# Kernel optimization log

Hardware: AMD Instinct MI355X
Metric: run time of the kernel (lower is better)

## Reference

```python
import jax, jax.numpy as jnp
import numpy as np

SEQ, BATCH, IN_DIM, HID, LAYERS, OUT = 512, 64, 512, 1024, 4, 1


def setup_inputs() -> dict:
    key = jax.random.key(0)
    ks = jax.random.split(key, 8)
    s = 1.0 / np.sqrt(HID)  # PyTorch default init range
    u = lambda k, shape: jax.random.uniform(k, shape, jnp.float32, -s, s)
    return {
        "x": jax.random.normal(ks[0], (SEQ, BATCH, IN_DIM), jnp.float32),
        "w_ih0": u(ks[1], (4 * HID, IN_DIM)),
        "w_ih_rest": u(ks[2], (LAYERS - 1, 4 * HID, HID)),
        "w_hh": u(ks[3], (LAYERS, 4 * HID, HID)),
        "b_ih": u(ks[4], (LAYERS, 4 * HID)),
        "b_hh": u(ks[5], (LAYERS, 4 * HID)),
        "fc_w": u(ks[6], (OUT, HID)),
        "fc_b": u(ks[7], (OUT,)),
    }


def _lstm_layer(xs, w_ih, w_hh, b):
    # xs: [T, B, D]; PyTorch gate order: i, f, g, o
    T, B, _ = xs.shape
    H = w_hh.shape[1]
    gx = jnp.einsum("tbd,gd->tbg", xs, w_ih) + b  # precompute input GEMM [T,B,4H]

    def step(carry, g_t):
        h, c = carry
        g = g_t + h @ w_hh.T
        i, f, gg, o = jnp.split(g, 4, axis=-1)
        c = jax.nn.sigmoid(f) * c + jax.nn.sigmoid(i) * jnp.tanh(gg)
        h = jax.nn.sigmoid(o) * jnp.tanh(c)
        return (h, c), h

    init = (jnp.zeros((B, H), xs.dtype), jnp.zeros((B, H), xs.dtype))
    _, hs = jax.lax.scan(step, init, gx)
    return hs  # [T, B, H]


def reference(x, w_ih0, w_ih_rest, w_hh, b_ih, b_hh, fc_w, fc_b):
    h = _lstm_layer(x, w_ih0, w_hh[0], b_ih[0] + b_hh[0])
    for l in range(1, LAYERS):
        h = _lstm_layer(h, w_ih_rest[l - 1], w_hh[l], b_ih[l] + b_hh[l])
    # Faithful to original: output is seq-first [T,B,H], and x[:, -1, :]
    # selects the LAST BATCH element over all timesteps -> [T, H]
    last = jax.nn.sigmoid(h[:, -1, :])
    return last @ fc_w.T + fc_b  # [T, OUT]
```

## Files before the change

### kernel.cpp

```cpp
#include <hip/hip_runtime.h>


typedef unsigned short u16;
typedef short bf16x8 __attribute__((ext_vector_type(8)));
typedef float f32x4 __attribute__((ext_vector_type(4)));
typedef float f32x16 __attribute__((ext_vector_type(16)));

__device__ __forceinline__ u16 f2bf(float f) {
  unsigned u = __float_as_uint(f);
  return (u16)((u + 0x7FFFu + ((u >> 16) & 1u)) >> 16);
}
__device__ __forceinline__ float bf2f(u16 s) {
  return __uint_as_float(((unsigned)s) << 16);
}
__device__ __forceinline__ bf16x8 ld8(const u16* p) {
  uint4 v = *(const uint4*)p;
  return __builtin_bit_cast(bf16x8, v);
}
__device__ __forceinline__ float sigf(float x) {
  x = fminf(fmaxf(x, -30.f), 30.f);
  return 1.f / (1.f + __expf(-x));
}
__device__ __forceinline__ float tanhf_(float x) {
  x = fminf(fmaxf(x, -15.f), 15.f);
  float e = __expf(-2.f * x);
  return (1.f - e) / (1.f + e);
}

#define AT_LD(p) __hip_atomic_load((p), __ATOMIC_RELAXED, __HIP_MEMORY_SCOPE_AGENT)
#define AT_ST(p, v) __hip_atomic_store((p), (v), __ATOMIC_RELAXED, __HIP_MEMORY_SCOPE_AGENT)

__global__ void repack_w(const float* __restrict__ wih0, const float* __restrict__ wihr,
                         const float* __restrict__ whh, u16* __restrict__ WCAT) {
  size_t i = (size_t)blockIdx.x * 256 + threadIdx.x;
  int l = (int)(i >> 23);
  int r = (int)(i >> 11) & 4095;
  int c = (int)i & 2047;
  int Kx = l ? 1024 : 512;
  float v = 0.f;
  if (c < Kx) v = l ? wihr[((size_t)(l - 1) * 4096 + r) * 1024 + c]
                    : wih0[(size_t)r * 512 + c];
  else if (c < Kx + 1024) v = whh[((size_t)l * 4096 + r) * 1024 + (c - Kx)];
  WCAT[i] = f2bf(v);
}

__global__ void repack_x(const float* __restrict__ x, u16* __restrict__ XP) {
  int i = blockIdx.x * 256 + threadIdx.x;
  int t = i >> 12, r = i & 4095, kc = r >> 6, b = r & 63;
  const float* src = x + ((size_t)t * 64 + b) * 512 + kc * 8;
  float4 v0 = *(const float4*)src, v1 = *(const float4*)(src + 4);
  u16 o[8] = {f2bf(v0.x), f2bf(v0.y), f2bf(v0.z), f2bf(v0.w),
              f2bf(v1.x), f2bf(v1.y), f2bf(v1.z), f2bf(v1.w)};
  *(uint4*)(XP + ((size_t)(t * 64 + kc) * 64 + b) * 8) = *(uint4*)o;
}

__global__ void bias_add(const float* __restrict__ a, const float* __restrict__ b,
                         float* __restrict__ o) {
  int i = blockIdx.x * blockDim.x + threadIdx.x;
  o[i] = a[i] + b[i];
}

template <int NF, int FX>
__device__ __forceinline__ void run_pipe(
    int layer, int w64, const u16* __restrict__ WCAT, const u16* __restrict__ XP,
    u16* __restrict__ HR, u16* __restrict__ HOUT, const float* __restrict__ BIAS,
    int* __restrict__ FLAG, float* R) {
  const int tid = threadIdx.x;
  const int lane = tid & 63, wv = tid >> 6;
  const int ks = wv & 3, nh = wv >> 2;
  const int l31 = lane & 31, lhi = lane >> 5;
  const int W = layer * 64 + w64;

  bf16x8 wf[NF];
  {
    const int lr = nh * 32 + l31;
    const int grow = (lr >> 4) * 1024 + 16 * w64 + (lr & 15);
    const u16* wrow = WCAT + ((size_t)layer * 4096 + grow) * 2048;
#pragma unroll
    for (int kk = 0; kk < NF; ++kk) {
      int f = ks * NF + kk;
      wf[kk] = ld8(wrow + f * 16 + lhi * 8);
    }
  }

  const int u = tid & 15, bp = tid >> 4;
  const int col = 16 * w64 + u;
  float c0 = 0.f, c1 = 0.f;
  const float bi = BIAS[layer * 4096 + col];
  const float bf_ = BIAS[layer * 4096 + 1024 + col];
  const float bg = BIAS[layer * 4096 + 2048 + col];
  const float bo = BIAS[layer * 4096 + 3072 + col];

  const int lane_base = (lhi * 64 + l31) * 8;
  u16* HRL = HR + (size_t)layer * 2097152;
  const u16* M0B = (NF == 32) ? HR + (size_t)(layer - 1) * 2097152 : XP;
  const int lrD = nh * 32 + l31;

  const bool needA = (layer > 0) && (ks * NF < FX);
  const bool needB = (ks * NF + NF > FX);
  const bool needC = (layer < 3);
  const int lm1 = (layer > 0) ? layer - 1 : layer;
  const int lp1 = (layer < 3) ? layer + 1 : layer;
  int* fA = FLAG + (lm1 * 64 + lane) * 64;
  int* fB = FLAG + (layer * 64 + lane) * 64;
  int* fC = FLAG + (lp1 * 64 + lane) * 64;
  const int NEVER = -0x40000000;

  *(f32x4*)&R[tid * 8] = f32x4{0.f, 0.f, 0.f, 0.f};
  *(f32x4*)&R[tid * 8 + 4] = f32x4{0.f, 0.f, 0.f, 0.f};
  __syncthreads();

  for (int t = 0; t < 512; ++t) {
    if (needC && (t & 7) == 0) {
      const int thC = t - 24;
      for (;;) {
        bool ok = AT_LD(fC) >= thC;
        if (__ballot(ok) == ~0ull) break;
      }
    }
    {
      const int thA = needA ? t + 1 : NEVER;
      const int thB = needB ? t : NEVER;
      for (;;) {
        bool ok = (AT_LD(fA) >= thA) & (AT_LD(fB) >= thB);
        if (__ballot(ok) == ~0ull) break;
      }
    }

    float* Rb = R + (t & 1) * 4096;
    const u16* P0 = M0B + ((NF == 32) ? (size_t)(t & 31) * 65536
                                      : (size_t)t * 32768) + lane_base;
    const u16* P1 = HRL + (size_t)((t - 1) & 31) * 65536 + lane_base - (size_t)FX * 1024;

    f32x16 acc0 = {}, acc1 = {};
    uint4 a0[8], a1[8];
#pragma unroll
    for (int p = 0; p < 8; ++p) {
      int f = ks * NF + p;
      const u16* ap = (f < FX ? P0 : P1) + (size_t)f * 1024;
      a0[p] = *(const uint4*)ap;
      a1[p] = *(const uint4*)(ap + 256);
    }
#pragma unroll
    for (int kk = 0; kk < NF; ++kk) {
      uint4 ca = a0[kk & 7], cb = a1[kk & 7];
      if (kk + 8 < NF) {
        int f = ks * NF + kk + 8;
        const u16* ap = (f < FX ? P0 : P1) + (size_t)f * 1024;
        a0[kk & 7] = *(const uint4*)ap;
        a1[kk & 7] = *(const uint4*)(ap + 256);
      }
      acc0 = __builtin_amdgcn_mfma_f32_32x32x16_bf16(
          __builtin_bit_cast(bf16x8, ca), wf[kk], acc0, 0, 0, 0);
      acc1 = __builtin_amdgcn_mfma_f32_32x32x16_bf16(
          __builtin_bit_cast(bf16x8, cb), wf[kk], acc1, 0, 0, 0);
    }
#pragma unroll
    for (int r = 0; r < 16; ++r) {
      int m = (r & 3) + 8 * (r >> 2) + 4 * lhi;
      atomicAdd(&Rb[m * 64 + lrD], acc0[r]);
      atomicAdd(&Rb[(32 + m) * 64 + lrD], acc1[r]);
    }
    __syncthreads();
    {
      float p0i = Rb[bp * 64 + u] + bi, p0f = Rb[bp * 64 + 16 + u] + bf_;
      float p0g = Rb[bp * 64 + 32 + u] + bg, p0o = Rb[bp * 64 + 48 + u] + bo;
      float p1i = Rb[(bp + 32) * 64 + u] + bi, p1f = Rb[(bp + 32) * 64 + 16 + u] + bf_;
      float p1g = Rb[(bp + 32) * 64 + 32 + u] + bg, p1o = Rb[(bp + 32) * 64 + 48 + u] + bo;
      c0 = sigf(p0f) * c0 + sigf(p0i) * tanhf_(p0g);
      float h0 = sigf(p0o) * tanhf_(c0);
      c1 = sigf(p1f) * c1 + sigf(p1i) * tanhf_(p1g);
      float h1 = sigf(p1o) * tanhf_(c1);
      u16 hb0 = f2bf(h0), hb1 = f2bf(h1);
      unsigned n0 = (unsigned)(u16)__shfl_down((int)(unsigned)hb0, 1, 64);
      unsigned n1 = (unsigned)(u16)__shfl_down((int)(unsigned)hb1, 1, 64);
      if ((u & 1) == 0) {
        unsigned pk0 = (unsigned)hb0 | (n0 << 16);
        unsigned pk1 = (unsigned)hb1 | (n1 << 16);
        u16* slot = HRL + (size_t)(t & 31) * 65536;
        size_t e0 = ((size_t)(col >> 3) * 64 + bp) * 8 + (col & 7);
        AT_ST((unsigned*)(slot + e0), pk0);
        AT_ST((unsigned*)(slot + e0 + 256), pk1);
        if (layer == 3 && bp == 31)
          *(unsigned*)(HOUT + (size_t)t * 1024 + col) = pk1;
      }
      float* Rn = R + ((t + 1) & 1) * 4096;
      *(f32x4*)&Rn[tid * 8] = f32x4{0.f, 0.f, 0.f, 0.f};
      *(f32x4*)&Rn[tid * 8 + 4] = f32x4{0.f, 0.f, 0.f, 0.f};
    }
    __syncthreads();
    if (tid == 0) AT_ST(&FLAG[W * 64], t + 1);
  }
}

__global__ __launch_bounds__(512, 2) void lstm_pipe(
    const u16* __restrict__ WCAT, const u16* __restrict__ XP,
    u16* __restrict__ HR, u16* __restrict__ HOUT,
    const float* __restrict__ BIAS, int* __restrict__ FLAG) {
  __shared__ float R[2 * 4096];
  const int w = blockIdx.x;
  const int layer = w >> 6, w64 = w & 63;
  if (layer == 0) run_pipe<24, 32>(0, w64, WCAT, XP, HR, HOUT, BIAS, FLAG, R);
  else            run_pipe<32, 64>(layer, w64, WCAT, XP, HR, HOUT, BIAS, FLAG, R);
}

__global__ void lstm_head(const u16* __restrict__ Hl, const float* __restrict__ fcw,
                          const float* __restrict__ fcb, float* __restrict__ out) {
  int t = blockIdx.x, tid = threadIdx.x;
  const u16* hrow = Hl + (size_t)t * 1024;
  float s = 0.f;
  for (int j = tid; j < 1024; j += 256)
    s += sigf(bf2f(hrow[j])) * fcw[j];
  for (int o = 32; o; o >>= 1) s += __shfl_down(s, o, 64);
  __shared__ float red[4];
  if ((tid & 63) == 0) red[tid >> 6] = s;
  __syncthreads();
  if (tid == 0) out[t] = red[0] + red[1] + red[2] + red[3] + fcb[0];
}

extern "C" void kernel_launch(void* const* d_in, const int* in_sizes, int n_in,
                              void* d_out, int out_size, void* d_ws, size_t ws_size,
                              hipStream_t stream) {
  const float* x    = (const float*)d_in[0];
  const float* wih0 = (const float*)d_in[1];
  const float* wihr = (const float*)d_in[2];
  const float* whh  = (const float*)d_in[3];
  const float* bih  = (const float*)d_in[4];
  const float* bhh  = (const float*)d_in[5];
  const float* fcw  = (const float*)d_in[6];
  const float* fcb  = (const float*)d_in[7];
  float* out = (float*)d_out;

  char* ws = (char*)d_ws;
  size_t off = 0;
  auto alc = [&](size_t b) { void* p = ws + off; off = (off + b + 255) & ~(size_t)255; return p; };
  u16* WCAT  = (u16*)alc(33554432ull * 2);
  u16* XP    = (u16*)alc(16777216ull * 2);
  u16* HR    = (u16*)alc(8388608ull * 2);
  u16* HOUT  = (u16*)alc(524288ull * 2);
  float* BIAS = (float*)alc(16384 * 4);
  int* FLAG  = (int*)alc(256 * 64 * 4);
  (void)ws_size; (void)in_sizes; (void)n_in; (void)out_size;

  hipMemsetAsync(HR, 0, 8388608ull * 2, stream);
  hipMemsetAsync(FLAG, 0, 256 * 64 * 4, stream);
  repack_w<<<dim3(131072), 256, 0, stream>>>(wih0, wihr, whh, WCAT);
  repack_x<<<dim3(8192), 256, 0, stream>>>(x, XP);
  bias_add<<<dim3(64), 256, 0, stream>>>(bih, bhh, BIAS);

  void* args[] = {&WCAT, &XP, &HR, &HOUT, &BIAS, &FLAG};
  hipLaunchCooperativeKernel((const void*)lstm_pipe, dim3(256), dim3(512),
                             args, 0, stream);

  lstm_head<<<dim3(512), 256, 0, stream>>>(HOUT, fcw, fcb, out);
}
```

Before: 15.10 ms.

## Narrow flag polling to only the producer blocks each K-slice depends on

Replaces the all-64-lanes flag wait with per-slice polling that checks only the producer flags covering the K range each wave consumes. The second half of the dependency is polled mid-loop after the first eight MFMAs, so early compute can start before every producer has finished. The downstream backpressure poll is now restricted to wave 0. This is meant to cut spin-wait latency and cross-block serialization in the persistent LSTM pipeline, at the risk of subtle ordering bugs if the offset mapping is wrong.

```diff
diff --git a/kernel.cpp b/kernel.cpp
--- a/kernel.cpp
+++ b/kernel.cpp
@@ -29,6 +29,14 @@
 
 #define AT_LD(p) __hip_atomic_load((p), __ATOMIC_RELAXED, __HIP_MEMORY_SCOPE_AGENT)
 #define AT_ST(p, v) __hip_atomic_store((p), (v), __ATOMIC_RELAXED, __HIP_MEMORY_SCOPE_AGENT)
+
+#define POLLW(PTR, CNT, THR)                                           \
+  if (CNT) {                                                           \
+    for (;;) {                                                         \
+      bool ok_ = (lane >= (CNT)) || (AT_LD(PTR) >= (THR));             \
+      if (__ballot(ok_) == ~0ull) break;                               \
+    }                                                                  \
+  }
 
 __global__ void repack_w(const float* __restrict__ wih0, const float* __restrict__ wihr,
                          const float* __restrict__ whh, u16* __restrict__ WCAT) {
@@ -96,36 +104,38 @@
   const u16* M0B = (NF == 32) ? HR + (size_t)(layer - 1) * 2097152 : XP;
   const int lrD = nh * 32 + l31;
 
-  const bool needA = (layer > 0) && (ks * NF < FX);
-  const bool needB = (ks * NF + NF > FX);
-  const bool needC = (layer < 3);
+  int ob0 = 0, oc0 = 0, ob1 = 0, oc1 = 0;
+  int ab0 = 0, ac0 = 0;
+  if (NF == 32) {
+    if (ks >= 2) { ob0 = (ks - 2) * 32; oc0 = 16; ob1 = ob0 + 16; oc1 = 16; }
+    else         { ab0 = 32 * ks; ac0 = 32; }
+  } else {
+    if (ks == 1)      { ob0 = 0;  oc0 = 16; }
+    else if (ks == 2) { ob0 = 16; oc0 = 16; ob1 = 32; oc1 = 8; }
+    else if (ks == 3) { ob0 = 40; oc0 = 16; ob1 = 56; oc1 = 8; }
+  }
   const int lm1 = (layer > 0) ? layer - 1 : layer;
   const int lp1 = (layer < 3) ? layer + 1 : layer;
-  int* fA = FLAG + (lm1 * 64 + lane) * 64;
-  int* fB = FLAG + (layer * 64 + lane) * 64;
-  int* fC = FLAG + (lp1 * 64 + lane) * 64;
-  const int NEVER = -0x40000000;
+  int* fBa = FLAG + ((size_t)layer * 64 + ob0 + lane) * 64;
+  int* fBb = FLAG + ((size_t)layer * 64 + ob1 + lane) * 64;
+  int* fAa = FLAG + ((size_t)lm1 * 64 + ab0 + lane) * 64;
+  int* fC  = FLAG + ((size_t)lp1 * 64 + lane) * 64;
+  const bool needC = (layer < 3);
 
   *(f32x4*)&R[tid * 8] = f32x4{0.f, 0.f, 0.f, 0.f};
   *(f32x4*)&R[tid * 8 + 4] = f32x4{0.f, 0.f, 0.f, 0.f};
   __syncthreads();
 
   for (int t = 0; t < 512; ++t) {
-    if (needC && (t & 7) == 0) {
+    if (needC && wv == 0 && (t & 7) == 0) {
       const int thC = t - 24;
       for (;;) {
         bool ok = AT_LD(fC) >= thC;
         if (__ballot(ok) == ~0ull) break;
       }
     }
-    {
-      const int thA = needA ? t + 1 : NEVER;
-      const int thB = needB ? t : NEVER;
-      for (;;) {
-        bool ok = (AT_LD(fA) >= thA) & (AT_LD(fB) >= thB);
-        if (__ballot(ok) == ~0ull) break;
-      }
-    }
+    POLLW(fAa, ac0, t + 1);
+    POLLW(fBa, oc0, t);
 
     float* Rb = R + (t & 1) * 4096;
     const u16* P0 = M0B + ((NF == 32) ? (size_t)(t & 31) * 65536
@@ -144,6 +154,7 @@
 #pragma unroll
     for (int kk = 0; kk < NF; ++kk) {
       uint4 ca = a0[kk & 7], cb = a1[kk & 7];
+      if (kk == 8) { POLLW(fBb, oc1, t); }
       if (kk + 8 < NF) {
         int f = ks * NF + kk + 8;
         const u16* ap = (f < FX ? P0 : P1) + (size_t)f * 1024;
```

New measurement: 15.44 ms. 1.02x slower.
